# Kernel tuning notes

Measured on AMD Instinct MI355X. Metric: run time of the kernel, lower is better.

Reference implementation:

```python
import jax, jax.numpy as jnp
import numpy as np

N = 100000   # nodes
E = 1000000  # edges
F_IN = 15    # node feature dim
H = 64       # hidden dim
EMB = 128    # embedding dim
R = 13       # relations
NB = 4       # bases


def _xavier(key, shape):
    fan_in, fan_out = shape[-2], shape[-1]
    lim = float(np.sqrt(6.0 / (fan_in + fan_out)))
    return jax.random.uniform(key, shape, jnp.float32, -lim, lim)


def setup_inputs() -> dict:
    key = jax.random.key(0)
    ks = jax.random.split(key, 24)
    inp = {}
    inp["node_features"] = jax.random.normal(ks[0], (N, F_IN), jnp.float32)
    inp["edge_index"] = jax.random.randint(ks[1], (2, E), 0, N, jnp.int32)
    inp["edge_type"] = jax.random.randint(ks[2], (E,), 0, R, jnp.int32)
    # input projection (15 -> 64)
    inp["W_in"] = _xavier(ks[3], (F_IN, H)); inp["b_in"] = jnp.zeros((H,), jnp.float32)
    # RGCN layer 0
    inp["Wself0"] = _xavier(ks[4], (H, H)); inp["bself0"] = jnp.zeros((H,), jnp.float32)
    inp["bases0"] = _xavier(ks[5], (NB, H, H))
    inp["coeffs0"] = _xavier(ks[6], (R, NB))
    # RGCN layer 1
    inp["Wself1"] = _xavier(ks[7], (H, H)); inp["bself1"] = jnp.zeros((H,), jnp.float32)
    inp["bases1"] = _xavier(ks[8], (NB, H, H))
    inp["coeffs1"] = _xavier(ks[9], (R, NB))
    # readout MLP (2H -> H -> EMB)
    inp["Wr1"] = _xavier(ks[10], (2 * H, H)); inp["br1"] = jnp.zeros((H,), jnp.float32)
    inp["Wr2"] = _xavier(ks[11], (H, EMB)); inp["br2"] = jnp.zeros((EMB,), jnp.float32)
    # node projection (H -> EMB)
    inp["Wnp"] = _xavier(ks[12], (H, EMB)); inp["bnp"] = jnp.zeros((EMB,), jnp.float32)
    return inp


def _rgcn_layer(h, src, tgt, etype, Wself, bself, bases, coeffs):
    # h: (N, H). Sum over relations of per-relation gather+matmul+scatter-add
    # == single scatter over all edges with per-edge relation weight.
    # Basis decomposition: W_r = sum_b coeffs[r,b] * bases[b].
    h_src = h[src]                 # (E, H) gather
    c_e = coeffs[etype]            # (E, NB) per-edge basis coefficients
    msg = jnp.zeros((h_src.shape[0], bases.shape[2]), h.dtype)
    for b in range(bases.shape[0]):  # fixed small loop over NB=4 bases
        msg = msg + c_e[:, b:b + 1] * (h_src @ bases[b])
    agg = jax.ops.segment_sum(msg, tgt, num_segments=h.shape[0])  # (N, H)
    # NOTE: original code computes degree norm but never applies it (dead code),
    # so aggregation is an unnormalized scatter-add, reproduced faithfully here.
    return jax.nn.relu(h @ Wself + bself + agg)  # dropout is identity in eval


def reference(node_features, edge_index, edge_type, W_in, b_in,
              Wself0, bself0, bases0, coeffs0,
              Wself1, bself1, bases1, coeffs1,
              Wr1, br1, Wr2, br2, Wnp, bnp):
    src, tgt = edge_index[0], edge_index[1]
    h = node_features @ W_in + b_in                      # (N, H)
    h = _rgcn_layer(h, src, tgt, edge_type, Wself0, bself0, bases0, coeffs0)
    h = _rgcn_layer(h, src, tgt, edge_type, Wself1, bself1, bases1, coeffs1)
    # graph readout: mean + max pooling over nodes -> MLP
    g = jnp.concatenate([h.mean(axis=0), h.max(axis=0)])  # (2H,)
    graph_emb = jax.nn.relu(g @ Wr1 + br1) @ Wr2 + br2    # (EMB,)
    node_emb = h @ Wnp + bnp                              # (N, EMB)
    return graph_emb, node_emb
```

## Files before the change

kernel.cpp:

```cpp
#include <hip/hip_runtime.h>
#include <hip/hip_bf16.h>

#define NN 100000
#define EE 1000000
#define FIN 15
#define HH 64
#define EMBD 128
#define RR 13
#define NBASE 4
#define NP 391
#define CAP 1700128
#define SENT (15 << 17)

typedef __hip_bfloat16 bf16;
typedef __attribute__((ext_vector_type(8))) short short8;
typedef __attribute__((ext_vector_type(4))) float f32x4;

__device__ __forceinline__ float b2f(bf16 x) { return __bfloat162float(x); }
__device__ __forceinline__ float bcast(float v, int l) {
    return __uint_as_float(__builtin_amdgcn_readlane(__float_as_uint(v), l));
}
__device__ __forceinline__ int bcasti(int v, int l) {
    return (int)__builtin_amdgcn_readlane((unsigned)v, l);
}
__device__ __forceinline__ unsigned short f2bu(float f) {
    bf16 t = __float2bfloat16(f);
    return *reinterpret_cast<unsigned short*>(&t);
}
__device__ __forceinline__ float bu2f(unsigned u) {
    return __uint_as_float(u << 16);
}

__global__ void k_detect(const void* __restrict__ win, int* __restrict__ flag) {
    int tid = threadIdx.x;
    const bf16* p = (const bf16*)win;
    int cnt = 0;
    for (int i = tid; i < FIN * HH; i += 64) {
        float v = b2f(p[i]);
        if (!(fabsf(v) < 0.3f)) cnt++;
    }
#pragma unroll
    for (int off = 32; off > 0; off >>= 1) cnt += __shfl_down(cnt, off, 64);
    if (tid == 0) *flag = (cnt > 40) ? 1 : 0;
}

struct ConvTab {
    const void* in[17];
    int n[17];
    int cum[18];
};

__global__ void k_convert_all(ConvTab tab, float* __restrict__ base,
                              const int* __restrict__ flag) {
    int g = blockIdx.x * 256 + threadIdx.x;
    if (g >= tab.cum[17]) return;
    int t = 0;
#pragma unroll
    for (int i = 0; i < 17; ++i) if (g >= tab.cum[i + 1]) t = i + 1;
    int local = g - tab.cum[t];
    if (local >= tab.n[t]) return;
    float v;
    if (*flag) v = ((const float*)tab.in[t])[local];
    else       v = b2f(((const bf16*)tab.in[t])[local]);
    base[g] = v;
}

__global__ void k_zero(int* __restrict__ a, int n) {
    int i = blockIdx.x * 256 + threadIdx.x;
    if (i < n) a[i] = 0;
}

__global__ void k_fill(int* __restrict__ a, int n, int val) {
    int i = blockIdx.x * 256 + threadIdx.x;
    if (i < n) a[i] = val;
}

__global__ void k_hist(const int* __restrict__ tgt, int* __restrict__ count,
                       int* __restrict__ rank) {
    int e = blockIdx.x * 256 + threadIdx.x;
    if (e >= EE) return;
    rank[e] = atomicAdd(&count[tgt[e]], 1);
}

__global__ void k_scan1(const int* __restrict__ count, int* __restrict__ scanned,
                        int* __restrict__ partials) {
    __shared__ int buf[256];
    int tid = threadIdx.x;
    int i = blockIdx.x * 256 + tid;
    int v = (i < NN) ? ((count[i] + 7) & ~7) : 0;
    buf[tid] = v;
    __syncthreads();
    for (int off = 1; off < 256; off <<= 1) {
        int t = (tid >= off) ? buf[tid - off] : 0;
        __syncthreads();
        buf[tid] += t;
        __syncthreads();
    }
    if (i < NN) scanned[i] = buf[tid] - v;
    if (tid == 255) partials[blockIdx.x] = buf[255];
}

__global__ void k_scan2(int* __restrict__ partials) {
    __shared__ int buf[512];
    int tid = threadIdx.x;
    int v = (tid < NP) ? partials[tid] : 0;
    buf[tid] = v;
    __syncthreads();
    for (int off = 1; off < 512; off <<= 1) {
        int t = (tid >= off) ? buf[tid - off] : 0;
        __syncthreads();
        buf[tid] += t;
        __syncthreads();
    }
    if (tid < NP) partials[tid] = buf[tid] - v;
}

__global__ void k_scatter(const int* __restrict__ src, const int* __restrict__ tgt,
                          const int* __restrict__ et, const int* __restrict__ rank,
                          const int* __restrict__ scanned, const int* __restrict__ partials,
                          int* __restrict__ packed) {
    int e = blockIdx.x * 256 + threadIdx.x;
    if (e >= EE) return;
    int t = tgt[e];
    int pos = scanned[t] + partials[t >> 8] + rank[e];
    packed[pos] = src[e] | (et[e] << 17);
}

__global__ void k_coef(const float* __restrict__ c0, const float* __restrict__ c1,
                       float* __restrict__ o0, float* __restrict__ o1) {
    int t = threadIdx.x;
    int r = t >> 2, b = t & 3;
    o0[t] = (r < RR) ? c0[r * NBASE + b] : 0.f;
    o1[t] = (r < RR) ? c1[r * NBASE + b] : 0.f;
}

__global__ void k_wcat(const float* __restrict__ bases0, const float* __restrict__ Wself0,
                       const float* __restrict__ bases1, const float* __restrict__ Wself1,
                       unsigned short* __restrict__ W0, unsigned short* __restrict__ W1) {
    int idx = blockIdx.x * 256 + threadIdx.x;
    if (idx >= HH * 320) return;
    int n = idx / 320, k = idx - n * 320;
    int b = k >> 6, kk = k & 63;
    float v0 = (b < 4) ? bases0[b * 4096 + kk * 64 + n] : Wself0[kk * 64 + n];
    float v1 = (b < 4) ? bases1[b * 4096 + kk * 64 + n] : Wself1[kk * 64 + n];
    W0[idx] = f2bu(v0);
    W1[idx] = f2bu(v1);
}

__global__ void k_wt(const float* __restrict__ Wnp, unsigned short* __restrict__ WT) {
    int idx = blockIdx.x * 256 + threadIdx.x;
    if (idx >= EMBD * HH) return;
    int c = idx >> 6, k = idx & 63;
    float w = Wnp[k * EMBD + c];
    unsigned short hi = f2bu(w);
    WT[idx] = hi;
    WT[EMBD * HH + idx] = f2bu(w - bu2f(hi));
}


__global__ void k_input_proj(const float* __restrict__ nf, const float* __restrict__ Win,
                             const float* __restrict__ bin, unsigned short* __restrict__ h) {
    __shared__ float w[FIN * HH];
    __shared__ float bb[HH];
    int tid = threadIdx.x;
    for (int i = tid; i < FIN * HH; i += 256) w[i] = Win[i];
    if (tid < HH) bb[tid] = bin[tid];
    __syncthreads();
    int idx = blockIdx.x * 256 + tid;
    if (idx >= NN * HH) return;
    int n = idx >> 6, j = idx & 63;
    float acc = bb[j];
    const float* row = nf + n * FIN;
#pragma unroll
    for (int k = 0; k < FIN; ++k) acc = fmaf(row[k], w[k * HH + j], acc);
    h[idx] = f2bu(acc);
}

__device__ __forceinline__ void edge_group16(const unsigned short* __restrict__ hin,
                                             const float* __restrict__ cc,
                                             int lane, int pk, int j, float S[4]) {
    float hv[16];
    int rr[16];
#pragma unroll
    for (int k = 0; k < 16; ++k) {
        int v = bcasti(pk, j + k);
        rr[k] = (v >> 17) & 0xF;
        hv[k] = bu2f((unsigned)hin[(v & 0x1FFFF) * HH + lane]);
    }
#pragma unroll
    for (int hh = 0; hh < 2; ++hh) {
        float4 cv[8];
#pragma unroll
        for (int k = 0; k < 8; ++k)
            cv[k] = *(const float4*)(cc + rr[hh * 8 + k] * 4);
#pragma unroll
        for (int k = 0; k < 8; ++k) {
            float hk = hv[hh * 8 + k];
            S[0] = fmaf(cv[k].x, hk, S[0]);
            S[1] = fmaf(cv[k].y, hk, S[1]);
            S[2] = fmaf(cv[k].z, hk, S[2]);
            S[3] = fmaf(cv[k].w, hk, S[3]);
        }
    }
}

__device__ __forceinline__ void edge_group8(const unsigned short* __restrict__ hin,
                                            const float* __restrict__ cc,
                                            int lane, int pk, int j, float S[4]) {
    float hv[8];
    int rr[8];
#pragma unroll
    for (int k = 0; k < 8; ++k) {
        int v = bcasti(pk, j + k);
        rr[k] = (v >> 17) & 0xF;
        hv[k] = bu2f((unsigned)hin[(v & 0x1FFFF) * HH + lane]);
    }
    float4 cv[8];
#pragma unroll
    for (int k = 0; k < 8; ++k) cv[k] = *(const float4*)(cc + rr[k] * 4);
#pragma unroll
    for (int k = 0; k < 8; ++k) {
        float hk = hv[k];
        S[0] = fmaf(cv[k].x, hk, S[0]);
        S[1] = fmaf(cv[k].y, hk, S[1]);
        S[2] = fmaf(cv[k].z, hk, S[2]);
        S[3] = fmaf(cv[k].w, hk, S[3]);
    }
}

__device__ __forceinline__ void gather_node(const unsigned short* __restrict__ hin,
                                            const int* __restrict__ packed,
                                            const float* __restrict__ cc,
                                            int lane, int pk, int s0, int cntp,
                                            float S[4]) {
    int lim = min(64, cntp);
    int j = 0;
    for (; j + 16 <= lim; j += 16) edge_group16(hin, cc, lane, pk, j, S);
    if (j < lim) edge_group8(hin, cc, lane, pk, j, S);
    for (int base = 64; base < cntp; base += 64) {
        int pkx = packed[s0 + base + lane];
        int lim2 = min(64, cntp - base);
        int j2 = 0;
        for (; j2 + 16 <= lim2; j2 += 16) edge_group16(hin, cc, lane, pkx, j2, S);
        if (j2 < lim2) edge_group8(hin, cc, lane, pkx, j2, S);
    }
}

__global__ void __launch_bounds__(256, 6)
k_layer(const unsigned short* __restrict__ hin, const int* __restrict__ packed,
        const int* __restrict__ count, const int* __restrict__ scanned,
        const int* __restrict__ partials, const float* __restrict__ cc,
        const unsigned short* __restrict__ Wc, const float* __restrict__ bself,
        unsigned short* __restrict__ hout) {
    __shared__ __align__(16) unsigned short Sb[16 * 264];
    int tid = threadIdx.x;
    int lane = tid & 63;
    int wv = tid >> 6;
    int t0 = blockIdx.x * 16;
    int nb = t0 + wv * 4;

    int4 c4  = *(const int4*)(count + nb);
    int4 sc4 = *(const int4*)(scanned + nb);
    int pb = partials[t0 >> 8];
    int s00 = sc4.x + pb, s01 = sc4.y + pb, s02 = sc4.z + pb, s03 = sc4.w + pb;
    int cp0 = (c4.x + 7) & ~7, cp1 = (c4.y + 7) & ~7;
    int cp2 = (c4.z + 7) & ~7, cp3 = (c4.w + 7) & ~7;

    int pk0 = packed[s00 + lane];
    int pk1 = packed[s01 + lane];
    int pk2 = packed[s02 + lane];
    int pk3 = packed[s03 + lane];

    float S0[4] = {0, 0, 0, 0}, S1[4] = {0, 0, 0, 0};
    float S2[4] = {0, 0, 0, 0}, S3[4] = {0, 0, 0, 0};
    gather_node(hin, packed, cc, lane, pk0, s00, cp0, S0);
    gather_node(hin, packed, cc, lane, pk1, s01, cp1, S1);
    gather_node(hin, packed, cc, lane, pk2, s02, cp2, S2);
    gather_node(hin, packed, cc, lane, pk3, s03, cp3, S3);

#pragma unroll
    for (int b = 0; b < NBASE; ++b) {
        Sb[(wv * 4 + 0) * 264 + b * 64 + lane] = f2bu(S0[b]);
        Sb[(wv * 4 + 1) * 264 + b * 64 + lane] = f2bu(S1[b]);
        Sb[(wv * 4 + 2) * 264 + b * 64 + lane] = f2bu(S2[b]);
        Sb[(wv * 4 + 3) * 264 + b * 64 + lane] = f2bu(S3[b]);
    }
    __syncthreads();

    int m16 = lane & 15;
    int g = lane >> 4;
    f32x4 acc = {0.f, 0.f, 0.f, 0.f};
    const unsigned short* brow = Wc + (wv * 16 + m16) * 320 + g * 8;
#pragma unroll
    for (int kb = 0; kb < 8; ++kb) {
        short8 a = *(const short8*)(&Sb[m16 * 264 + kb * 32 + g * 8]);
        short8 b = *(const short8*)(brow + kb * 32);
        acc = __builtin_amdgcn_mfma_f32_16x16x32_bf16(a, b, acc, 0, 0, 0);
    }
    const unsigned short* hrow = hin + (t0 + m16) * HH + g * 8;
#pragma unroll
    for (int kb = 0; kb < 2; ++kb) {
        short8 a = *(const short8*)(hrow + kb * 32);
        short8 b = *(const short8*)(brow + 256 + kb * 32);
        acc = __builtin_amdgcn_mfma_f32_16x16x32_bf16(a, b, acc, 0, 0, 0);
    }
    int col = wv * 16 + m16;
    float bias = bself[col];
#pragma unroll
    for (int r = 0; r < 4; ++r) {
        int row = g * 4 + r;
        hout[(t0 + row) * HH + col] = f2bu(fmaxf(acc[r] + bias, 0.f));
    }
}

__global__ void k_reduce(const unsigned short* __restrict__ h, float* __restrict__ psum,
                         float* __restrict__ pmax) {
    __shared__ float ls[256], lm[256];
    int tid = threadIdx.x;
    int j = tid & 63;
    int slot = tid >> 6;
    float s = 0.f, m = -1e30f;
    for (int n = blockIdx.x * 4 + slot; n < NN; n += gridDim.x * 4) {
        float v = bu2f((unsigned)h[n * HH + j]);
        s += v;
        m = fmaxf(m, v);
    }
    ls[tid] = s; lm[tid] = m;
    __syncthreads();
    if (tid < 64) {
        s = ls[tid] + ls[tid + 64] + ls[tid + 128] + ls[tid + 192];
        m = fmaxf(fmaxf(lm[tid], lm[tid + 64]), fmaxf(lm[tid + 128], lm[tid + 192]));
        psum[blockIdx.x * 64 + tid] = s;
        pmax[blockIdx.x * 64 + tid] = m;
    }
}

__global__ void k_finish(const float* __restrict__ psum, const float* __restrict__ pmax,
                         const float* __restrict__ Wr1, const float* __restrict__ br1,
                         const float* __restrict__ Wr2, const float* __restrict__ br2,
                         void* __restrict__ out, const int* __restrict__ flag) {
    __shared__ float ls[256], lm[256];
    __shared__ float g[2 * HH];
    __shared__ float tbuf[HH];
    int tid = threadIdx.x;
    int j = tid & 63;
    int slot = tid >> 6;
    float s = 0.f, m = -1e30f;
    for (int i = slot; i < 256; i += 4) {
        s += psum[i * 64 + j];
        m = fmaxf(m, pmax[i * 64 + j]);
    }
    ls[tid] = s; lm[tid] = m;
    __syncthreads();
    if (tid < 64) {
        s = ls[tid] + ls[tid + 64] + ls[tid + 128] + ls[tid + 192];
        m = fmaxf(fmaxf(lm[tid], lm[tid + 64]), fmaxf(lm[tid + 128], lm[tid + 192]));
        g[tid] = s * (1.0f / NN);
        g[64 + tid] = m;
    }
    __syncthreads();
    if (tid < 64) {
        float acc = br1[tid];
#pragma unroll 8
        for (int k = 0; k < 2 * HH; ++k) acc = fmaf(g[k], Wr1[k * HH + tid], acc);
        tbuf[tid] = fmaxf(acc, 0.f);
    }
    __syncthreads();
    if (tid < EMBD) {
        float acc = br2[tid];
#pragma unroll 8
        for (int k = 0; k < HH; ++k) acc = fmaf(tbuf[k], Wr2[k * EMBD + tid], acc);
        if (*flag) ((float*)out)[tid] = acc;
        else       ((bf16*)out)[tid] = __float2bfloat16(acc);
    }
}

__global__ void __launch_bounds__(256, 8)
k_node_emb2(const unsigned short* __restrict__ h, const unsigned short* __restrict__ WT,
            const float* __restrict__ bnp, void* __restrict__ out,
            const int* __restrict__ flag) {
    int tid = threadIdx.x;
    int lane = tid & 63;
    int wv = tid >> 6;
    int n0 = blockIdx.x * 16;
    int m16 = lane & 15, g = lane >> 4;

    const unsigned short* arow = h + (n0 + m16) * HH + g * 8;
    short8 a0 = *(const short8*)(arow);
    short8 a1 = *(const short8*)(arow + 32);

    int c0 = wv * 32;
    const unsigned short* bp0 = WT + (c0 + m16) * HH + g * 8;
    const unsigned short* bp1 = WT + (c0 + 16 + m16) * HH + g * 8;
    const unsigned short* lp0 = bp0 + EMBD * HH;
    const unsigned short* lp1 = bp1 + EMBD * HH;

    f32x4 accA = {0.f, 0.f, 0.f, 0.f}, accB = {0.f, 0.f, 0.f, 0.f};
    accA = __builtin_amdgcn_mfma_f32_16x16x32_bf16(a0, *(const short8*)bp0, accA, 0, 0, 0);
    accA = __builtin_amdgcn_mfma_f32_16x16x32_bf16(a1, *(const short8*)(bp0 + 32), accA, 0, 0, 0);
    accA = __builtin_amdgcn_mfma_f32_16x16x32_bf16(a0, *(const short8*)lp0, accA, 0, 0, 0);
    accA = __builtin_amdgcn_mfma_f32_16x16x32_bf16(a1, *(const short8*)(lp0 + 32), accA, 0, 0, 0);
    accB = __builtin_amdgcn_mfma_f32_16x16x32_bf16(a0, *(const short8*)bp1, accB, 0, 0, 0);
    accB = __builtin_amdgcn_mfma_f32_16x16x32_bf16(a1, *(const short8*)(bp1 + 32), accB, 0, 0, 0);
    accB = __builtin_amdgcn_mfma_f32_16x16x32_bf16(a0, *(const short8*)lp1, accB, 0, 0, 0);
    accB = __builtin_amdgcn_mfma_f32_16x16x32_bf16(a1, *(const short8*)(lp1 + 32), accB, 0, 0, 0);

    float biasA = bnp[c0 + m16], biasB = bnp[c0 + 16 + m16];
    if (*flag) {
        float* o = (float*)out + EMBD;
#pragma unroll
        for (int r = 0; r < 4; ++r) {
            long node = n0 + g * 4 + r;
            o[node * EMBD + c0 + m16]      = accA[r] + biasA;
            o[node * EMBD + c0 + 16 + m16] = accB[r] + biasB;
        }
    } else {
        bf16* o = (bf16*)out + EMBD;
#pragma unroll
        for (int r = 0; r < 4; ++r) {
            long node = n0 + g * 4 + r;
            o[node * EMBD + c0 + m16]      = __float2bfloat16(accA[r] + biasA);
            o[node * EMBD + c0 + 16 + m16] = __float2bfloat16(accB[r] + biasB);
        }
    }
}

extern "C" void kernel_launch(void* const* d_in, const int* in_sizes, int n_in,
                              void* d_out, int out_size, void* d_ws, size_t ws_size,
                              hipStream_t stream) {
    const int* eidx  = (const int*)d_in[1];
    const int* etype = (const int*)d_in[2];
    const int* src = eidx;
    const int* tgt = eidx + EE;

    int* flag = (int*)d_ws;
    float* base = (float*)d_ws + 16;

    const int fidx[17] = {0, 3, 4, 5, 6, 7, 8, 9, 10, 11, 12, 13, 14, 15, 16, 17, 18};
    ConvTab tab;
    float* conv[19];
    int cum = 0;
    for (int t = 0; t < 17; ++t) {
        int i = fidx[t];
        tab.in[t] = d_in[i];
        tab.n[t] = in_sizes[i];
        tab.cum[t] = cum;
        conv[i] = base + cum;
        cum += (in_sizes[i] + 15) & ~15;
    }
    tab.cum[17] = cum;

    k_detect<<<1, 64, 0, stream>>>(d_in[3], flag);
    k_convert_all<<<(cum + 255) / 256, 256, 0, stream>>>(tab, base, flag);

    float* p = base + cum;
    float* psum = p;  p += 256 * 64;
    float* pmax = p;  p += 256 * 64;
    float* c16a = p;  p += 64;
    float* c16b = p;  p += 64;
    int* count    = (int*)p;           p += NN;
    int* scanned  = (int*)p;           p += NN;
    int* partials = (int*)p;           p += 512;
    int* rank     = (int*)p;           p += EE;
    int* packed   = (int*)p;           p += CAP;
    unsigned short* hbf0 = (unsigned short*)p;
    unsigned short* hbf1 = hbf0 + (size_t)NN * HH;
    unsigned short* Wc0  = hbf1 + (size_t)NN * HH;
    unsigned short* Wc1  = Wc0 + HH * 320;
    unsigned short* WT   = Wc1 + HH * 320;

    const float* nf      = conv[0];
    const float* Win     = conv[3];
    const float* bin     = conv[4];
    const float* Wself0  = conv[5];
    const float* bself0  = conv[6];
    const float* bases0  = conv[7];
    const float* coeffs0 = conv[8];
    const float* Wself1  = conv[9];
    const float* bself1  = conv[10];
    const float* bases1  = conv[11];
    const float* coeffs1 = conv[12];
    const float* Wr1     = conv[13];
    const float* br1     = conv[14];
    const float* Wr2     = conv[15];
    const float* br2     = conv[16];
    const float* Wnp     = conv[17];
    const float* bnp     = conv[18];

    const int NHB = (NN * HH) / 256;
    const int LYB = NN / 16;
    const int EB  = (EE + 255) / 256;

    k_zero<<<(NN + 255) / 256, 256, 0, stream>>>(count, NN);
    k_fill<<<(CAP + 255) / 256, 256, 0, stream>>>(packed, CAP, SENT);
    k_hist<<<EB, 256, 0, stream>>>(tgt, count, rank);
    k_scan1<<<NP, 256, 0, stream>>>(count, scanned, partials);
    k_scan2<<<1, 512, 0, stream>>>(partials);
    k_scatter<<<EB, 256, 0, stream>>>(src, tgt, etype, rank, scanned, partials, packed);

    k_coef<<<1, 64, 0, stream>>>(coeffs0, coeffs1, c16a, c16b);
    k_wcat<<<(HH * 320 + 255) / 256, 256, 0, stream>>>(bases0, Wself0, bases1, Wself1, Wc0, Wc1);
    k_wt<<<(EMBD * HH + 255) / 256, 256, 0, stream>>>(Wnp, WT);
    k_input_proj<<<NHB, 256, 0, stream>>>(nf, Win, bin, hbf0);

    k_layer<<<LYB, 256, 0, stream>>>(hbf0, packed, count, scanned, partials, c16a, Wc0, bself0, hbf1);
    k_layer<<<LYB, 256, 0, stream>>>(hbf1, packed, count, scanned, partials, c16b, Wc1, bself1, hbf0);

    k_reduce<<<256, 256, 0, stream>>>(hbf0, psum, pmax);
    k_finish<<<1, 256, 0, stream>>>(psum, pmax, Wr1, br1, Wr2, br2, d_out, flag);
    k_node_emb2<<<LYB, 256, 0, stream>>>(hbf0, WT, bnp, d_out, flag);
}
```

Before: 425.2 us.

## Fuse node projection and pooling partials into second RGCN layer epilogue

The second layer kernel now stages its bf16 ReLU output tile in shared memory, runs the H->EMB node projection MFMAs directly on it, and writes per-block sum/max partials. This removes the separate node-embedding and node-reduction kernels, which re-read the whole hidden-state array from global memory. A new small reduce kernel folds the per-block partials. The layer-1 kernel gains extra syncs, registers and work in its tail, which may lower occupancy during the gather phase.

Measured after the change: 392.8 us. 7.6% less time.

```diff
diff --git a/kernel.cpp b/kernel.cpp
--- a/kernel.cpp
+++ b/kernel.cpp
@@ -11,6 +11,7 @@
 #define NP 391
 #define CAP 1700128
 #define SENT (15 << 17)
+#define LYB (NN / 16)
 
 typedef __hip_bfloat16 bf16;
 typedef __attribute__((ext_vector_type(8))) short short8;
@@ -246,12 +247,16 @@
     }
 }
 
+template <int TAIL>
 __global__ void __launch_bounds__(256, 6)
 k_layer(const unsigned short* __restrict__ hin, const int* __restrict__ packed,
         const int* __restrict__ count, const int* __restrict__ scanned,
         const int* __restrict__ partials, const float* __restrict__ cc,
         const unsigned short* __restrict__ Wc, const float* __restrict__ bself,
-        unsigned short* __restrict__ hout) {
+        unsigned short* __restrict__ hout,
+        const unsigned short* __restrict__ WT, const float* __restrict__ bnp,
+        void* __restrict__ out, const int* __restrict__ flag,
+        float* __restrict__ psum, float* __restrict__ pmax) {
     __shared__ __align__(16) unsigned short Sb[16 * 264];
     int tid = threadIdx.x;
     int lane = tid & 63;
@@ -306,32 +311,91 @@
     }
     int col = wv * 16 + m16;
     float bias = bself[col];
-#pragma unroll
-    for (int r = 0; r < 4; ++r) {
-        int row = g * 4 + r;
-        hout[(t0 + row) * HH + col] = f2bu(fmaxf(acc[r] + bias, 0.f));
-    }
-}
-
-__global__ void k_reduce(const unsigned short* __restrict__ h, float* __restrict__ psum,
-                         float* __restrict__ pmax) {
+
+    if (TAIL == 0) {
+#pragma unroll
+        for (int r = 0; r < 4; ++r) {
+            int row = g * 4 + r;
+            hout[(t0 + row) * HH + col] = f2bu(fmaxf(acc[r] + bias, 0.f));
+        }
+        return;
+    }
+
+    __syncthreads();
+#pragma unroll
+    for (int r = 0; r < 4; ++r)
+        Sb[(g * 4 + r) * 264 + col] = f2bu(fmaxf(acc[r] + bias, 0.f));
+    __syncthreads();
+
+    const unsigned short* ar = &Sb[m16 * 264 + g * 8];
+    short8 a0 = *(const short8*)(ar);
+    short8 a1 = *(const short8*)(ar + 32);
+    int c0 = wv * 32;
+    const unsigned short* bp0 = WT + (c0 + m16) * HH + g * 8;
+    const unsigned short* bp1 = WT + (c0 + 16 + m16) * HH + g * 8;
+    const unsigned short* lp0 = bp0 + EMBD * HH;
+    const unsigned short* lp1 = bp1 + EMBD * HH;
+
+    f32x4 eA = {0.f, 0.f, 0.f, 0.f}, eB = {0.f, 0.f, 0.f, 0.f};
+    eA = __builtin_amdgcn_mfma_f32_16x16x32_bf16(a0, *(const short8*)bp0, eA, 0, 0, 0);
+    eA = __builtin_amdgcn_mfma_f32_16x16x32_bf16(a1, *(const short8*)(bp0 + 32), eA, 0, 0, 0);
+    eA = __builtin_amdgcn_mfma_f32_16x16x32_bf16(a0, *(const short8*)lp0, eA, 0, 0, 0);
+    eA = __builtin_amdgcn_mfma_f32_16x16x32_bf16(a1, *(const short8*)(lp0 + 32), eA, 0, 0, 0);
+    eB = __builtin_amdgcn_mfma_f32_16x16x32_bf16(a0, *(const short8*)bp1, eB, 0, 0, 0);
+    eB = __builtin_amdgcn_mfma_f32_16x16x32_bf16(a1, *(const short8*)(bp1 + 32), eB, 0, 0, 0);
+    eB = __builtin_amdgcn_mfma_f32_16x16x32_bf16(a0, *(const short8*)lp1, eB, 0, 0, 0);
+    eB = __builtin_amdgcn_mfma_f32_16x16x32_bf16(a1, *(const short8*)(lp1 + 32), eB, 0, 0, 0);
+
+    float biasA = bnp[c0 + m16], biasB = bnp[c0 + 16 + m16];
+    if (*flag) {
+        float* o = (float*)out + EMBD;
+#pragma unroll
+        for (int r = 0; r < 4; ++r) {
+            long node = t0 + g * 4 + r;
+            o[node * EMBD + c0 + m16]      = eA[r] + biasA;
+            o[node * EMBD + c0 + 16 + m16] = eB[r] + biasB;
+        }
+    } else {
+        bf16* o = (bf16*)out + EMBD;
+#pragma unroll
+        for (int r = 0; r < 4; ++r) {
+            long node = t0 + g * 4 + r;
+            o[node * EMBD + c0 + m16]      = __float2bfloat16(eA[r] + biasA);
+            o[node * EMBD + c0 + 16 + m16] = __float2bfloat16(eB[r] + biasB);
+        }
+    }
+
+    if (wv == 0) {
+        float s = 0.f, m = -1e30f;
+#pragma unroll
+        for (int r16 = 0; r16 < 16; ++r16) {
+            float v = bu2f((unsigned)Sb[r16 * 264 + lane]);
+            s += v;
+            m = fmaxf(m, v);
+        }
+        psum[blockIdx.x * 64 + lane] = s;
+        pmax[blockIdx.x * 64 + lane] = m;
+    }
+}
+
+__global__ void k_reduce2(const float* __restrict__ psum, const float* __restrict__ pmax,
+                          float* __restrict__ psum2, float* __restrict__ pmax2) {
     __shared__ float ls[256], lm[256];
     int tid = threadIdx.x;
     int j = tid & 63;
     int slot = tid >> 6;
     float s = 0.f, m = -1e30f;
-    for (int n = blockIdx.x * 4 + slot; n < NN; n += gridDim.x * 4) {
-        float v = bu2f((unsigned)h[n * HH + j]);
-        s += v;
-        m = fmaxf(m, v);
+    for (int n = blockIdx.x * 4 + slot; n < LYB; n += 256 * 4) {
+        s += psum[n * 64 + j];
+        m = fmaxf(m, pmax[n * 64 + j]);
     }
     ls[tid] = s; lm[tid] = m;
     __syncthreads();
     if (tid < 64) {
         s = ls[tid] + ls[tid + 64] + ls[tid + 128] + ls[tid + 192];
         m = fmaxf(fmaxf(lm[tid], lm[tid + 64]), fmaxf(lm[tid + 128], lm[tid + 192]));
-        psum[blockIdx.x * 64 + tid] = s;
-        pmax[blockIdx.x * 64 + tid] = m;
+        psum2[blockIdx.x * 64 + tid] = s;
+        pmax2[blockIdx.x * 64 + tid] = m;
     }
 }
 
@@ -372,56 +436,6 @@
         for (int k = 0; k < HH; ++k) acc = fmaf(tbuf[k], Wr2[k * EMBD + tid], acc);
         if (*flag) ((float*)out)[tid] = acc;
         else       ((bf16*)out)[tid] = __float2bfloat16(acc);
-    }
-}
-
-__global__ void __launch_bounds__(256, 8)
-k_node_emb2(const unsigned short* __restrict__ h, const unsigned short* __restrict__ WT,
-            const float* __restrict__ bnp, void* __restrict__ out,
-            const int* __restrict__ flag) {
-    int tid = threadIdx.x;
-    int lane = tid & 63;
-    int wv = tid >> 6;
-    int n0 = blockIdx.x * 16;
-    int m16 = lane & 15, g = lane >> 4;
-
-    const unsigned short* arow = h + (n0 + m16) * HH + g * 8;
-    short8 a0 = *(const short8*)(arow);
-    short8 a1 = *(const short8*)(arow + 32);
-
-    int c0 = wv * 32;
-    const unsigned short* bp0 = WT + (c0 + m16) * HH + g * 8;
-    const unsigned short* bp1 = WT + (c0 + 16 + m16) * HH + g * 8;
-    const unsigned short* lp0 = bp0 + EMBD * HH;
-    const unsigned short* lp1 = bp1 + EMBD * HH;
-
-    f32x4 accA = {0.f, 0.f, 0.f, 0.f}, accB = {0.f, 0.f, 0.f, 0.f};
-    accA = __builtin_amdgcn_mfma_f32_16x16x32_bf16(a0, *(const short8*)bp0, accA, 0, 0, 0);
-    accA = __builtin_amdgcn_mfma_f32_16x16x32_bf16(a1, *(const short8*)(bp0 + 32), accA, 0, 0, 0);
-    accA = __builtin_amdgcn_mfma_f32_16x16x32_bf16(a0, *(const short8*)lp0, accA, 0, 0, 0);
-    accA = __builtin_amdgcn_mfma_f32_16x16x32_bf16(a1, *(const short8*)(lp0 + 32), accA, 0, 0, 0);
-    accB = __builtin_amdgcn_mfma_f32_16x16x32_bf16(a0, *(const short8*)bp1, accB, 0, 0, 0);
-    accB = __builtin_amdgcn_mfma_f32_16x16x32_bf16(a1, *(const short8*)(bp1 + 32), accB, 0, 0, 0);
-    accB = __builtin_amdgcn_mfma_f32_16x16x32_bf16(a0, *(const short8*)lp1, accB, 0, 0, 0);
-    accB = __builtin_amdgcn_mfma_f32_16x16x32_bf16(a1, *(const short8*)(lp1 + 32), accB, 0, 0, 0);
-
-    float biasA = bnp[c0 + m16], biasB = bnp[c0 + 16 + m16];
-    if (*flag) {
-        float* o = (float*)out + EMBD;
-#pragma unroll
-        for (int r = 0; r < 4; ++r) {
-            long node = n0 + g * 4 + r;
-            o[node * EMBD + c0 + m16]      = accA[r] + biasA;
-            o[node * EMBD + c0 + 16 + m16] = accB[r] + biasB;
-        }
-    } else {
-        bf16* o = (bf16*)out + EMBD;
-#pragma unroll
-        for (int r = 0; r < 4; ++r) {
-            long node = n0 + g * 4 + r;
-            o[node * EMBD + c0 + m16]      = __float2bfloat16(accA[r] + biasA);
-            o[node * EMBD + c0 + 16 + m16] = __float2bfloat16(accB[r] + biasB);
-        }
     }
 }
 
@@ -454,8 +468,10 @@
     k_convert_all<<<(cum + 255) / 256, 256, 0, stream>>>(tab, base, flag);
 
     float* p = base + cum;
-    float* psum = p;  p += 256 * 64;
-    float* pmax = p;  p += 256 * 64;
+    float* psum  = p;  p += LYB * 64;
+    float* pmax  = p;  p += LYB * 64;
+    float* psum2 = p;  p += 256 * 64;
+    float* pmax2 = p;  p += 256 * 64;
     float* c16a = p;  p += 64;
     float* c16b = p;  p += 64;
     int* count    = (int*)p;           p += NN;
@@ -488,7 +504,6 @@
     const float* bnp     = conv[18];
 
     const int NHB = (NN * HH) / 256;
-    const int LYB = NN / 16;
     const int EB  = (EE + 255) / 256;
 
     k_zero<<<(NN + 255) / 256, 256, 0, stream>>>(count, NN);
@@ -503,10 +518,11 @@
     k_wt<<<(EMBD * HH + 255) / 256, 256, 0, stream>>>(Wnp, WT);
     k_input_proj<<<NHB, 256, 0, stream>>>(nf, Win, bin, hbf0);
 
-    k_layer<<<LYB, 256, 0, stream>>>(hbf0, packed, count, scanned, partials, c16a, Wc0, bself0, hbf1);
-    k_layer<<<LYB, 256, 0, stream>>>(hbf1, packed, count, scanned, partials, c16b, Wc1, bself1, hbf0);
-
-    k_reduce<<<256, 256, 0, stream>>>(hbf0, psum, pmax);
-    k_finish<<<1, 256, 0, stream>>>(psum, pmax, Wr1, br1, Wr2, br2, d_out, flag);
-    k_node_emb2<<<LYB, 256, 0, stream>>>(hbf0, WT, bnp, d_out, flag);
-}
+    k_layer<0><<<LYB, 256, 0, stream>>>(hbf0, packed, count, scanned, partials, c16a, Wc0, bself0,
+                                        hbf1, nullptr, nullptr, nullptr, nullptr, nullptr, nullptr);
+    k_layer<1><<<LYB, 256, 0, stream>>>(hbf1, packed, count, scanned, partials, c16b, Wc1, bself1,
+                                        hbf0, WT, bnp, d_out, flag, psum, pmax);
+
+    k_reduce2<<<256, 256, 0, stream>>>(psum, pmax, psum2, pmax2);
+    k_finish<<<1, 256, 0, stream>>>(psum2, pmax2, Wr1, br1, Wr2, br2, d_out, flag);
+}
```
